# Kernel tuning notes

Measured on AMD Instinct MI355X. Metric: run time of the kernel, lower is better.

Reference implementation:

```python
import jax, jax.numpy as jnp
import numpy as np

B, L, H, V = 64, 8, 4096, 50257


def setup_inputs() -> dict:
    key = jax.random.key(0)
    ks = jax.random.split(key, 5)
    return {
        "embedding": jax.random.normal(ks[0], (V, H), jnp.float32) * 0.02,
        "hidden_states": jax.random.normal(ks[1], (B, L, H), jnp.float32),
        "output_position": 7,  # scalar index of the position to sample from
        "temperatures": jax.random.uniform(ks[2], (B,), jnp.float32, 0.5, 1.5),
        "top_ps": jax.random.uniform(ks[3], (B,), jnp.float32, 0.7, 1.0),
        "tops_ks": jax.random.randint(ks[4], (B,), 1, 64),  # top-k in [1,64)
        "embedding_bias": jnp.zeros((V,), jnp.float32),
    }


def reference(embedding, hidden_states, output_position, temperatures, top_ps, tops_ks, embedding_bias):
    # select the output position: [B, H]
    h = hidden_states[:, output_position, :]
    # logits GEMM against tied embedding: [B, V]
    logits = jnp.einsum("bh,vh->bv", h, embedding) + embedding_bias[None, :]
    logits = logits / temperatures[:, None]
    probs = jax.nn.softmax(logits.astype(jnp.float32), axis=-1)

    # descending sort of probabilities
    order = jnp.argsort(-probs, axis=-1)                       # [B, V]
    probs_sort = jnp.take_along_axis(probs, order, axis=-1)    # [B, V]

    # top-p mask: exclusive cumulative sum exceeding top_p
    cum = jnp.cumsum(probs_sort, axis=-1)
    topp_mask = (cum - probs_sort) > top_ps[:, None]
    # top-k mask: rank >= k
    ranks = jnp.arange(V, dtype=tops_ks.dtype)[None, :]
    topk_mask = ranks >= tops_ks[:, None]

    probs_sort = jnp.where(topp_mask | topk_mask, 0.0, probs_sort)
    probs_sort = probs_sort / jnp.sum(probs_sort, axis=-1, keepdims=True)

    # scatter back to original vocab order via inverse permutation
    inv = jnp.argsort(order, axis=-1)
    probs_final = jnp.take_along_axis(probs_sort, inv, axis=-1)  # [B, V]

    # multinomial sampling (1 sample per row)
    logp = jnp.where(probs_final > 0, jnp.log(jnp.maximum(probs_final, 1e-38)), -jnp.inf)
    next_token_ids = jax.random.categorical(jax.random.key(42), logp, axis=-1)
    return next_token_ids
```

## Files before the change

kernel.cpp:

```cpp
#include <hip/hip_runtime.h>
#include <stdint.h>
#include <float.h>
#include <limits.h>


typedef __bf16 bf16x8 __attribute__((ext_vector_type(8)));
typedef float  f32x4  __attribute__((ext_vector_type(4)));

#define BN 64
#define BK 64

__device__ __forceinline__ void split8(const float* f, uint4& hi, uint4& lo) {
    bf16x8 vh, vl;
#pragma unroll
    for (int e = 0; e < 8; ++e) {
        const __bf16 h = (__bf16)f[e];
        vh[e] = h;
        vl[e] = (__bf16)(f[e] - (float)h);
    }
    hi = __builtin_bit_cast(uint4, vh);
    lo = __builtin_bit_cast(uint4, vl);
}

__global__ __launch_bounds__(256) void prep_h(
    const float* __restrict__ hs, const int* __restrict__ pos_p,
    unsigned short* __restrict__ Ahi, unsigned short* __restrict__ Alo,
    int H, int L)
{
    const int pos = pos_p[0];
    const int tid = blockIdx.x * 256 + threadIdx.x;
    const int b     = tid >> 8;
    const int kbase = (tid & 255) * 16;
    const float* src = hs + ((size_t)b * L + pos) * H + kbase;
    float f[16];
    *(float4*)&f[0]  = *(const float4*)(src);
    *(float4*)&f[4]  = *(const float4*)(src + 4);
    *(float4*)&f[8]  = *(const float4*)(src + 8);
    *(float4*)&f[12] = *(const float4*)(src + 12);

    const int r16 = b >> 4, ll = b & 15;
    const int kc  = kbase >> 5;
    const int lh0 = (kbase >> 3) & 3;
#pragma unroll
    for (int c = 0; c < 2; ++c) {
        uint4 hi, lo;
        split8(f + 8 * c, hi, lo);
        const size_t dst = ((size_t)(r16 * 128 + kc) * 64 + (lh0 + c) * 16 + ll) * 8;
        *(uint4*)&Ahi[dst] = hi;
        *(uint4*)&Alo[dst] = lo;
    }
}

__global__ __launch_bounds__(256) void logits_mfma(
    const float* __restrict__ emb,
    const unsigned short* __restrict__ Ahi,
    const unsigned short* __restrict__ Alo,
    const float* __restrict__ temps,
    const float* __restrict__ bias,
    float*       __restrict__ out,
    int V, int H)
{
    __shared__ unsigned short sBhi[2][64 * 64];
    __shared__ unsigned short sBlo[2][64 * 64];

    const int tid = threadIdx.x;
    const int v0  = blockIdx.x * BN;

    const int brow = tid >> 2;
    const int bcol = (tid & 3) * 16;

    const int lane  = tid & 63;
    const int w     = tid >> 6;
    const int rbase = (w >> 1) * 32;
    const int cbase = (w & 1) * 32;

    int offB[2][2];
#pragma unroll
    for (int j = 0; j < 2; ++j) {
        const int rb = cbase + 16 * j + (lane & 15);
#pragma unroll
        for (int ks = 0; ks < 2; ++ks) {
            const int ke = 32 * ks + (lane >> 4) * 8;
            offB[j][ks] = rb * 64 + (ke ^ ((rb & 7) * 8));
        }
    }
    const int wswz  = (brow & 7) * 8;
    const int woff0 = brow * 64 + (bcol ^ wswz);
    const int woff1 = brow * 64 + ((bcol + 8) ^ wswz);

    size_t abase[2];
#pragma unroll
    for (int i = 0; i < 2; ++i)
        abase[i] = (size_t)((w >> 1) * 2 + i) * 65536
                 + (size_t)(lane >> 4) * 128 + (size_t)(lane & 15) * 8;

    const int vglob = v0 + brow;
    const float* bsrc = emb + (size_t)vglob * H + bcol;

    float4 pf[4];
    auto issueB = [&](int k0) {
        if (vglob < V) {
#pragma unroll
            for (int q = 0; q < 4; ++q)
                pf[q] = *(const float4*)(bsrc + k0 + 4 * q);
        } else {
#pragma unroll
            for (int q = 0; q < 4; ++q)
                pf[q] = make_float4(0.f, 0.f, 0.f, 0.f);
        }
    };
    auto stageB = [&](int buf) {
        float f[16];
        *(float4*)&f[0]  = pf[0];
        *(float4*)&f[4]  = pf[1];
        *(float4*)&f[8]  = pf[2];
        *(float4*)&f[12] = pf[3];
        uint4 h0, l0, h1, l1;
        split8(f,     h0, l0);
        split8(f + 8, h1, l1);
        *(uint4*)&sBhi[buf][woff0] = h0;
        *(uint4*)&sBlo[buf][woff0] = l0;
        *(uint4*)&sBhi[buf][woff1] = h1;
        *(uint4*)&sBlo[buf][woff1] = l1;
    };

    f32x4 acc[2][2];
#pragma unroll
    for (int i = 0; i < 2; ++i)
#pragma unroll
        for (int j = 0; j < 2; ++j)
            acc[i][j] = (f32x4){0.f, 0.f, 0.f, 0.f};

    issueB(0);
    stageB(0);
    int cur = 0;
    for (int k0 = 0; k0 < H; k0 += BK) {
        __syncthreads();
        const bool more = (k0 + BK) < H;
        if (more) issueB(k0 + BK);

        const int kc = k0 >> 5;
        bf16x8 fah[2][2], fal[2][2];
#pragma unroll
        for (int i = 0; i < 2; ++i)
#pragma unroll
            for (int ks = 0; ks < 2; ++ks) {
                const size_t ai = abase[i] + (size_t)(kc + ks) * 512;
                fah[i][ks] = *(const bf16x8*)&Ahi[ai];
                fal[i][ks] = *(const bf16x8*)&Alo[ai];
            }
#pragma unroll
        for (int j = 0; j < 2; ++j) {
            bf16x8 fbh[2], fbl[2];
#pragma unroll
            for (int ks = 0; ks < 2; ++ks) {
                fbh[ks] = *(const bf16x8*)&sBhi[cur][offB[j][ks]];
                fbl[ks] = *(const bf16x8*)&sBlo[cur][offB[j][ks]];
            }
#pragma unroll
            for (int i = 0; i < 2; ++i)
#pragma unroll
                for (int ks = 0; ks < 2; ++ks) {
                    acc[i][j] = __builtin_amdgcn_mfma_f32_16x16x32_bf16(
                        fal[i][ks], fbh[ks], acc[i][j], 0, 0, 0);
                    acc[i][j] = __builtin_amdgcn_mfma_f32_16x16x32_bf16(
                        fah[i][ks], fbl[ks], acc[i][j], 0, 0, 0);
                    acc[i][j] = __builtin_amdgcn_mfma_f32_16x16x32_bf16(
                        fah[i][ks], fbh[ks], acc[i][j], 0, 0, 0);
                }
        }
        if (more) stageB(cur ^ 1);
        cur ^= 1;
    }

#pragma unroll
    for (int i = 0; i < 2; ++i)
#pragma unroll
        for (int j = 0; j < 2; ++j) {
            const int vv = v0 + cbase + 16 * j + (lane & 15);
            if (vv < V) {
                const float bv = bias[vv];
#pragma unroll
                for (int r = 0; r < 4; ++r) {
                    const int b = rbase + 16 * i + (lane >> 4) * 4 + r;
                    out[(size_t)b * V + vv] = (acc[i][j][r] + bv) / temps[b];
                }
            }
        }
}

__device__ __forceinline__ uint32_t rotl32(uint32_t x, int d) {
    return (x << d) | (x >> (32 - d));
}

__device__ float jax_gumbel(uint32_t flat) {
    const uint32_t k0 = 0u, k1 = 42u;
    const uint32_t ks[3] = { k0, k1, k0 ^ k1 ^ 0x1BD11BDAu };
    uint32_t x0 = 0u   + ks[0];
    uint32_t x1 = flat + ks[1];
    const int rot[2][4] = { {13, 15, 26, 6}, {17, 29, 16, 24} };
#pragma unroll
    for (int r = 0; r < 5; ++r) {
        const int* rr = rot[r & 1];
#pragma unroll
        for (int j = 0; j < 4; ++j) {
            x0 += x1;
            x1 = rotl32(x1, rr[j]);
            x1 ^= x0;
        }
        x0 += ks[(r + 1) % 3];
        x1 += ks[(r + 2) % 3] + (uint32_t)(r + 1);
    }
    const uint32_t bits = x0 ^ x1;
    const uint32_t fb = (bits >> 9) | 0x3F800000u;
    const float f = __uint_as_float(fb) - 1.0f;
    const float tiny = 1.17549435e-38f;
    float u = __fadd_rn(__fmul_rn(f, 1.0f), tiny);
    u = fmaxf(tiny, u);
    const float l1 = logf(u);
    return -logf(-l1);
}

#define NBINS 4096
#define CAP   2048
#define NKEEP 64

__global__ __launch_bounds__(256) void sample_kernel(
    const float* __restrict__ logits,
    const float* __restrict__ top_ps,
    const int*   __restrict__ top_ks,
    int*         __restrict__ out_ids,
    int V)
{
    const int b = blockIdx.x;
    const int tid = threadIdx.x;
    const float* row = logits + (size_t)b * V;

    __shared__ float swred[4];
    __shared__ int   bins[NBINS];
    __shared__ int   schunk[256];
    __shared__ int   sThrBin, sCnt, sMkeep;
    __shared__ float cval[CAP];
    __shared__ int   cidx[CAP];
    __shared__ float tval[NKEEP];
    __shared__ int   tidxs[NKEEP];

    float m = -INFINITY;
    for (int k = tid; k < V; k += 256) m = fmaxf(m, row[k]);
#pragma unroll
    for (int o = 32; o > 0; o >>= 1) m = fmaxf(m, __shfl_xor(m, o, 64));
    if ((tid & 63) == 0) swred[tid >> 6] = m;
    __syncthreads();
    m = fmaxf(fmaxf(swred[0], swred[1]), fmaxf(swred[2], swred[3]));

    for (int k = tid; k < NBINS; k += 256) bins[k] = 0;
    if (tid == 0) sCnt = 0;
    __syncthreads();

    float s = 0.f;
    for (int k = tid; k < V; k += 256) {
        const float x = row[k];
        s += expf(x - m);
        const float g = m - x;
        int bin = (int)(g * 256.0f);
        if (bin >= NBINS) bin = NBINS - 1;
        atomicAdd(&bins[bin], 1);
    }
#pragma unroll
    for (int o = 32; o > 0; o >>= 1) s += __shfl_xor(s, o, 64);
    __syncthreads();
    if ((tid & 63) == 0) swred[tid >> 6] = s;

    int csum = 0;
#pragma unroll
    for (int k = 0; k < NBINS / 256; ++k) csum += bins[tid * (NBINS / 256) + k];
    schunk[tid] = csum;
    __syncthreads();
    s = swred[0] + swred[1] + swred[2] + swred[3];
    if (tid == 0) {
        int cum = 0, chunk = 255;
        for (int c = 0; c < 256; ++c) {
            if (cum + schunk[c] >= NKEEP) { chunk = c; break; }
            cum += schunk[c];
        }
        int t = NBINS - 1;
        const int base = chunk * (NBINS / 256);
        for (int k = base; k < base + NBINS / 256; ++k) {
            cum += bins[k];
            if (cum >= NKEEP) { t = k; break; }
        }
        sThrBin = t;
    }
    __syncthreads();
    const int thrBin = sThrBin;

    for (int k = tid; k < V; k += 256) {
        const float x = row[k];
        const float g = m - x;
        int bin = (int)(g * 256.0f);
        if (bin >= NBINS) bin = NBINS - 1;
        if (bin <= thrBin) {
            const int p = atomicAdd(&sCnt, 1);
            if (p < CAP) { cval[p] = x; cidx[p] = k; }
        }
    }
    __syncthreads();
    const int C = min(sCnt, CAP);

    for (int i = tid; i < C; i += 256) {
        const float vi = cval[i];
        const int   ii = cidx[i];
        int rank = 0;
        for (int j = 0; j < C; ++j) {
            const float vj = cval[j];
            const int   ij = cidx[j];
            rank += (vj > vi) || (vj == vi && ij < ii);
        }
        if (rank < NKEEP) { tval[rank] = vi; tidxs[rank] = ii; }
    }
    __syncthreads();

    if (tid == 0) {
        const float pb = top_ps[b];
        const int   kk = top_ks[b];
        const int   nk = min(NKEEP, C);
        float cum = 0.f;
        int mk = 0;
        for (int r = 0; r < nk; ++r) {
            const float pr = expf(tval[r] - m) / s;
            cum += pr;
            const float excl = cum - pr;
            if (excl > pb || r >= kk) break;
            ++mk;
        }
        sMkeep = (mk > 0) ? mk : 1;
    }
    __syncthreads();
    const int mkeep = sMkeep;

    if (tid < 64) {
        float sc = -INFINITY;
        int vid = INT_MAX;
        if (tid < mkeep) {
            const int v = tidxs[tid];
            vid = v;
            sc = tval[tid] + jax_gumbel((uint32_t)b * (uint32_t)V + (uint32_t)v);
        }
#pragma unroll
        for (int o = 32; o > 0; o >>= 1) {
            const float os = __shfl_xor(sc, o, 64);
            const int   ov = __shfl_xor(vid, o, 64);
            if (os > sc || (os == sc && ov < vid)) { sc = os; vid = ov; }
        }
        if (tid == 0) out_ids[b] = vid;
    }
}

extern "C" void kernel_launch(void* const* d_in, const int* in_sizes, int n_in,
                              void* d_out, int out_size, void* d_ws, size_t ws_size,
                              hipStream_t stream)
{
    const float* emb   = (const float*)d_in[0];
    const float* hs    = (const float*)d_in[1];
    const int*   pos   = (const int*)d_in[2];
    const float* temps = (const float*)d_in[3];
    const float* tps   = (const float*)d_in[4];
    const int*   tks   = (const int*)d_in[5];
    const float* bias  = (const float*)d_in[6];

    const int B = in_sizes[3];
    const int V = in_sizes[6];
    const int H = (int)((long long)in_sizes[0] / V);
    const int L = (int)((long long)in_sizes[1] / ((long long)B * H));

    float*          logits = (float*)d_ws;
    unsigned short* Ahi    = (unsigned short*)((char*)d_ws + (16u << 20));
    unsigned short* Alo    = Ahi + (size_t)B * H;

    prep_h<<<(B * H) / (16 * 256), 256, 0, stream>>>(hs, pos, Ahi, Alo, H, L);

    const int nblk = (V + BN - 1) / BN;
    logits_mfma<<<nblk, 256, 0, stream>>>(emb, Ahi, Alo, temps, bias,
                                          logits, V, H);

    sample_kernel<<<B, 256, 0, stream>>>(logits, tps, tks, (int*)d_out, V);
}
```

Baseline: 354.7 us.

## Load embedding fragments straight to registers and software-pipeline the logits GEMM

Drops the shared-memory staging and block-wide barriers in the logits GEMM. Each wave now owns 32 vocab columns across all 64 batch rows and loads embedding rows directly into registers in MFMA fragment order, splitting them into bf16 hi/lo there. A four-deep register ring for B and double-buffered A loads overlap global latency with MFMA work. This removes LDS traffic and synchronisation on a memory-bound GEMM, at the cost of higher register pressure and less coalesced per-lane 32-byte row loads.

```diff
diff --git a/kernel.cpp b/kernel.cpp
--- a/kernel.cpp
+++ b/kernel.cpp
@@ -7,17 +7,17 @@
 typedef __bf16 bf16x8 __attribute__((ext_vector_type(8)));
 typedef float  f32x4  __attribute__((ext_vector_type(4)));
 
-#define BN 64
-#define BK 64
-
+__device__ __forceinline__ void split8v(const float* f, bf16x8& hi, bf16x8& lo) {
+#pragma unroll
+    for (int e = 0; e < 8; ++e) {
+        const __bf16 h = (__bf16)f[e];
+        hi[e] = h;
+        lo[e] = (__bf16)(f[e] - (float)h);
+    }
+}
 __device__ __forceinline__ void split8(const float* f, uint4& hi, uint4& lo) {
     bf16x8 vh, vl;
-#pragma unroll
-    for (int e = 0; e < 8; ++e) {
-        const __bf16 h = (__bf16)f[e];
-        vh[e] = h;
-        vl[e] = (__bf16)(f[e] - (float)h);
-    }
+    split8v(f, vh, vl);
     hi = __builtin_bit_cast(uint4, vh);
     lo = __builtin_bit_cast(uint4, vl);
 }
@@ -60,133 +60,109 @@
     float*       __restrict__ out,
     int V, int H)
 {
-    __shared__ unsigned short sBhi[2][64 * 64];
-    __shared__ unsigned short sBlo[2][64 * 64];
-
-    const int tid = threadIdx.x;
-    const int v0  = blockIdx.x * BN;
-
-    const int brow = tid >> 2;
-    const int bcol = (tid & 3) * 16;
-
-    const int lane  = tid & 63;
-    const int w     = tid >> 6;
-    const int rbase = (w >> 1) * 32;
-    const int cbase = (w & 1) * 32;
-
-    int offB[2][2];
-#pragma unroll
-    for (int j = 0; j < 2; ++j) {
-        const int rb = cbase + 16 * j + (lane & 15);
-#pragma unroll
-        for (int ks = 0; ks < 2; ++ks) {
-            const int ke = 32 * ks + (lane >> 4) * 8;
-            offB[j][ks] = rb * 64 + (ke ^ ((rb & 7) * 8));
-        }
-    }
-    const int wswz  = (brow & 7) * 8;
-    const int woff0 = brow * 64 + (bcol ^ wswz);
-    const int woff1 = brow * 64 + ((bcol + 8) ^ wswz);
-
-    size_t abase[2];
-#pragma unroll
-    for (int i = 0; i < 2; ++i)
-        abase[i] = (size_t)((w >> 1) * 2 + i) * 65536
-                 + (size_t)(lane >> 4) * 128 + (size_t)(lane & 15) * 8;
-
-    const int vglob = v0 + brow;
-    const float* bsrc = emb + (size_t)vglob * H + bcol;
-
-    float4 pf[4];
-    auto issueB = [&](int k0) {
-        if (vglob < V) {
-#pragma unroll
-            for (int q = 0; q < 4; ++q)
-                pf[q] = *(const float4*)(bsrc + k0 + 4 * q);
-        } else {
-#pragma unroll
-            for (int q = 0; q < 4; ++q)
-                pf[q] = make_float4(0.f, 0.f, 0.f, 0.f);
-        }
-    };
-    auto stageB = [&](int buf) {
-        float f[16];
-        *(float4*)&f[0]  = pf[0];
-        *(float4*)&f[4]  = pf[1];
-        *(float4*)&f[8]  = pf[2];
-        *(float4*)&f[12] = pf[3];
-        uint4 h0, l0, h1, l1;
-        split8(f,     h0, l0);
-        split8(f + 8, h1, l1);
-        *(uint4*)&sBhi[buf][woff0] = h0;
-        *(uint4*)&sBlo[buf][woff0] = l0;
-        *(uint4*)&sBhi[buf][woff1] = h1;
-        *(uint4*)&sBlo[buf][woff1] = l1;
-    };
-
-    f32x4 acc[2][2];
-#pragma unroll
-    for (int i = 0; i < 2; ++i)
+    const int tid  = threadIdx.x;
+    const int lane = tid & 63;
+    const int w    = tid >> 6;
+    const int wv0  = blockIdx.x * 128 + w * 32;
+
+    const int ll = lane & 15;
+    const int lh = lane >> 4;
+
+    const int NKC = H >> 5;
+
+    const float* bptr[2];
+#pragma unroll
+    for (int n = 0; n < 2; ++n) {
+        int r = wv0 + 16 * n + ll;
+        r = (r < V) ? r : (V - 1);
+        bptr[n] = emb + (size_t)r * H + lh * 8;
+    }
+
+    const size_t aoff = (size_t)lh * 128 + (size_t)ll * 8;
+
+    float4 rb[4][4];
+    bf16x8 aih[2][4], ail[2][4];
+    f32x4  acc[4][2];
+#pragma unroll
+    for (int i = 0; i < 4; ++i)
 #pragma unroll
         for (int j = 0; j < 2; ++j)
             acc[i][j] = (f32x4){0.f, 0.f, 0.f, 0.f};
 
-    issueB(0);
-    stageB(0);
-    int cur = 0;
-    for (int k0 = 0; k0 < H; k0 += BK) {
-        __syncthreads();
-        const bool more = (k0 + BK) < H;
-        if (more) issueB(k0 + BK);
-
-        const int kc = k0 >> 5;
-        bf16x8 fah[2][2], fal[2][2];
-#pragma unroll
-        for (int i = 0; i < 2; ++i)
-#pragma unroll
-            for (int ks = 0; ks < 2; ++ks) {
-                const size_t ai = abase[i] + (size_t)(kc + ks) * 512;
-                fah[i][ks] = *(const bf16x8*)&Ahi[ai];
-                fal[i][ks] = *(const bf16x8*)&Alo[ai];
-            }
-#pragma unroll
-        for (int j = 0; j < 2; ++j) {
-            bf16x8 fbh[2], fbl[2];
-#pragma unroll
-            for (int ks = 0; ks < 2; ++ks) {
-                fbh[ks] = *(const bf16x8*)&sBhi[cur][offB[j][ks]];
-                fbl[ks] = *(const bf16x8*)&sBlo[cur][offB[j][ks]];
-            }
-#pragma unroll
-            for (int i = 0; i < 2; ++i)
-#pragma unroll
-                for (int ks = 0; ks < 2; ++ks) {
-                    acc[i][j] = __builtin_amdgcn_mfma_f32_16x16x32_bf16(
-                        fal[i][ks], fbh[ks], acc[i][j], 0, 0, 0);
-                    acc[i][j] = __builtin_amdgcn_mfma_f32_16x16x32_bf16(
-                        fah[i][ks], fbl[ks], acc[i][j], 0, 0, 0);
-                    acc[i][j] = __builtin_amdgcn_mfma_f32_16x16x32_bf16(
-                        fah[i][ks], fbh[ks], acc[i][j], 0, 0, 0);
-                }
-        }
-        if (more) stageB(cur ^ 1);
-        cur ^= 1;
-    }
-
-#pragma unroll
-    for (int i = 0; i < 2; ++i)
-#pragma unroll
-        for (int j = 0; j < 2; ++j) {
-            const int vv = v0 + cbase + 16 * j + (lane & 15);
-            if (vv < V) {
-                const float bv = bias[vv];
+#define LOADB(t, bi) do {                                                     \
+    if ((t) < NKC) {                                                          \
+        _Pragma("unroll")                                                     \
+        for (int n = 0; n < 2; ++n) {                                         \
+            _Pragma("unroll")                                                 \
+            for (int q = 0; q < 2; ++q)                                       \
+                rb[bi][n * 2 + q] =                                           \
+                    *(const float4*)(bptr[n] + (size_t)(t) * 32 + q * 4);     \
+        }                                                                     \
+    }                                                                         \
+} while (0)
+
+#define LOADA(t, p) do {                                                      \
+    if ((t) < NKC) {                                                          \
+        _Pragma("unroll")                                                     \
+        for (int i = 0; i < 4; ++i) {                                         \
+            const size_t ai = aoff + (size_t)i * 65536 + (size_t)(t) * 512;   \
+            aih[p][i] = *(const bf16x8*)&Ahi[ai];                             \
+            ail[p][i] = *(const bf16x8*)&Alo[ai];                             \
+        }                                                                     \
+    }                                                                         \
+} while (0)
+
+#define COMPUTE(bi, p) do {                                                   \
+    bf16x8 fbh[2], fbl[2];                                                    \
+    _Pragma("unroll")                                                         \
+    for (int n = 0; n < 2; ++n) {                                             \
+        float f[8];                                                           \
+        *(float4*)&f[0] = rb[bi][2 * n];                                      \
+        *(float4*)&f[4] = rb[bi][2 * n + 1];                                  \
+        split8v(f, fbh[n], fbl[n]);                                           \
+    }                                                                         \
+    _Pragma("unroll")                                                         \
+    for (int j = 0; j < 2; ++j)                                               \
+        _Pragma("unroll")                                                     \
+        for (int i = 0; i < 4; ++i) {                                         \
+            acc[i][j] = __builtin_amdgcn_mfma_f32_16x16x32_bf16(              \
+                ail[p][i], fbh[j], acc[i][j], 0, 0, 0);                       \
+            acc[i][j] = __builtin_amdgcn_mfma_f32_16x16x32_bf16(              \
+                aih[p][i], fbl[j], acc[i][j], 0, 0, 0);                       \
+            acc[i][j] = __builtin_amdgcn_mfma_f32_16x16x32_bf16(              \
+                aih[p][i], fbh[j], acc[i][j], 0, 0, 0);                       \
+        }                                                                     \
+} while (0)
+
+    LOADA(0, 0);
+    LOADB(0, 0);
+    LOADB(1, 1);
+    LOADB(2, 2);
+
+    for (int kb = 0; kb < NKC; kb += 4) {
+        LOADB(kb + 3, 3); LOADA(kb + 1, 1); COMPUTE(0, 0);
+        LOADB(kb + 4, 0); LOADA(kb + 2, 0); COMPUTE(1, 1);
+        LOADB(kb + 5, 1); LOADA(kb + 3, 1); COMPUTE(2, 0);
+        LOADB(kb + 6, 2); LOADA(kb + 4, 0); COMPUTE(3, 1);
+    }
+#undef LOADB
+#undef LOADA
+#undef COMPUTE
+
+#pragma unroll
+    for (int j = 0; j < 2; ++j) {
+        const int vv = wv0 + 16 * j + ll;
+        if (vv < V) {
+            const float bv = bias[vv];
+#pragma unroll
+            for (int i = 0; i < 4; ++i)
 #pragma unroll
                 for (int r = 0; r < 4; ++r) {
-                    const int b = rbase + 16 * i + (lane >> 4) * 4 + r;
+                    const int b = 16 * i + lh * 4 + r;
                     out[(size_t)b * V + vv] = (acc[i][j][r] + bv) / temps[b];
                 }
-            }
-        }
+        }
+    }
 }
 
 __device__ __forceinline__ uint32_t rotl32(uint32_t x, int d) {
@@ -379,7 +355,7 @@
 
     prep_h<<<(B * H) / (16 * 256), 256, 0, stream>>>(hs, pos, Ahi, Alo, H, L);
 
-    const int nblk = (V + BN - 1) / BN;
+    const int nblk = (V + 127) / 128;
     logits_mfma<<<nblk, 256, 0, stream>>>(emb, Ahi, Alo, temps, bias,
                                           logits, V, H);
 
```

Result: slower. 377.2 us (+6.4%).
